# Kernel optimization log

Measured on AMD Instinct MI355X. Metric: run time of the kernel, lower is better.

The kernel has to match this reference:

```python
import jax, jax.numpy as jnp
import numpy as np

HEADS = 16
HEAD_DIM = 64  # qk_dim(1024) // heads(16)
SCALE = HEAD_DIM ** (-0.5)


def setup_inputs() -> dict:
    key = jax.random.key(0)
    k1, k2, k3, k4 = jax.random.split(key, 4)
    b, n, d = 2, 2048, 1024
    x = jax.random.normal(k1, (b, n, d), dtype=jnp.float32)
    mask = jax.random.randint(k2, (1, 1, n, n), 0, 2, dtype=jnp.int32)
    W_qkv = jax.random.normal(k3, (d, 3 * d), dtype=jnp.float32) * (d ** -0.5)
    W_out = jax.random.normal(k4, (d, d), dtype=jnp.float32) * (d ** -0.5)
    b_out = jnp.zeros((d,), dtype=jnp.float32)
    return {"x": x, "mask": mask, "W_qkv": W_qkv, "W_out": W_out, "b_out": b_out}


def reference(x, mask, W_qkv, W_out, b_out):
    b, n, d = x.shape
    qkv = x @ W_qkv  # [b, n, 3d]
    q, k, v = jnp.split(qkv, 3, axis=-1)

    def to_heads(t):
        return t.reshape(b, n, HEADS, HEAD_DIM).transpose(0, 2, 1, 3)  # b h n d

    q, k, v = to_heads(q), to_heads(k), to_heads(v)
    attn = jnp.einsum('bhid,bhjd->bhij', q, k) * SCALE
    attn = jnp.where(mask == 0, jnp.float32(-1e9), attn)
    attn = jax.nn.softmax(attn, axis=-1)
    out = jnp.einsum('bhij,bhjd->bhid', attn, v)  # b h n d
    out = out.transpose(0, 2, 1, 3).reshape(b, n, d)  # b n (h d)
    return out @ W_out + b_out
```

## Files before the change

kernel.cpp:

```cpp
#include <hip/hip_runtime.h>
#include <hip/hip_bf16.h>

typedef __bf16 bf16x8 __attribute__((ext_vector_type(8)));
typedef float f32x4 __attribute__((ext_vector_type(4)));
typedef float f32x16 __attribute__((ext_vector_type(16)));
typedef unsigned short u16;
typedef unsigned int u32;
typedef unsigned long long u64;
typedef u32 u32x4v __attribute__((ext_vector_type(4)));

#define QSCALE 0.18033688011112042f

__device__ __forceinline__ u16 f2b(float x) {
  __hip_bfloat16 h = __float2bfloat16(x);
  return __builtin_bit_cast(u16, h);
}

__device__ __forceinline__ float exp2_fast(float x) {
#if __has_builtin(__builtin_amdgcn_exp2f)
  return __builtin_amdgcn_exp2f(x);
#else
  float r; asm("v_exp_f32 %0, %1" : "=v"(r) : "v"(x)); return r;
#endif
}

__device__ __forceinline__ void gload_lds16(const void* g, void* l) {
  __builtin_amdgcn_global_load_lds((const __attribute__((address_space(1))) u32*)g,
                                   (__attribute__((address_space(3))) u32*)l, 16, 0, 0);
}

__global__ __launch_bounds__(256) void cast_bf16_kernel(const float* __restrict__ src,
                                                        u16* __restrict__ dst, int n4) {
  int i = blockIdx.x * 256 + threadIdx.x;
  if (i >= n4) return;
  float4 v = ((const float4*)src)[i];
  ushort4 o;
  o.x = f2b(v.x); o.y = f2b(v.y); o.z = f2b(v.z); o.w = f2b(v.w);
  ((ushort4*)dst)[i] = o;
}

__global__ __launch_bounds__(256) void transpose_cast_kernel(const float* __restrict__ src,
                                                             u16* __restrict__ dst,
                                                             int R, int C) {
  __shared__ float t[32][33];
  int c0 = blockIdx.x * 32, r0 = blockIdx.y * 32;
  int tx = threadIdx.x, ty = threadIdx.y;
  for (int k = 0; k < 32; k += 8)
    t[ty + k][tx] = src[(size_t)(r0 + ty + k) * C + c0 + tx];
  __syncthreads();
  for (int k = 0; k < 32; k += 8)
    dst[(size_t)(c0 + ty + k) * R + r0 + tx] = f2b(t[tx][ty + k]);
}

__global__ __launch_bounds__(256) void maskbits_kernel(const int* __restrict__ mask,
                                                       u64* __restrict__ bits) {
  int gtid = blockIdx.x * 256 + threadIdx.x;
  int wid = gtid >> 6, lane = gtid & 63;
  int v = mask[(size_t)wid * 64 + lane];
  u64 b = __ballot(v != 0);
  if (lane == 0) bits[wid] = b;
}

__global__ __launch_bounds__(256) void gemm_qkv_kernel(const u16* __restrict__ A,
                                                       const u16* __restrict__ Bt,
                                                       u16* __restrict__ Qb,
                                                       u16* __restrict__ Kb,
                                                       u16* __restrict__ Vt) {
  __shared__ u16 lA[128 * 32], lB[128 * 32];
  const int tid = threadIdx.x, lane = tid & 63, w = tid >> 6;
  const int wr = w >> 1, wc = w & 1, lrow = lane & 15, lk = lane >> 4;
  const int bm = blockIdx.y, bn = blockIdx.x;
  const int srow = tid >> 2, scol = (tid & 3) * 8;
  const u16* Arow = A + (size_t)(bm * 128 + srow) * 1024 + scol;
  const u16* Brow = Bt + (size_t)(bn * 128 + srow) * 1024 + scol;
  f32x4 acc[4][4] = {};
  for (int k0 = 0; k0 < 1024; k0 += 32) {
    __syncthreads();
    gload_lds16(Arow + k0,             (char*)lA + w * 1024);
    gload_lds16(Arow + 64 * 1024 + k0, (char*)lA + 4096 + w * 1024);
    gload_lds16(Brow + k0,             (char*)lB + w * 1024);
    gload_lds16(Brow + 64 * 1024 + k0, (char*)lB + 4096 + w * 1024);
    __syncthreads();
    bf16x8 af[4], bfr[4];
    for (int mi = 0; mi < 4; mi++)
      af[mi] = *(const bf16x8*)&lA[(wr * 64 + mi * 16 + lrow) * 32 + lk * 8];
    for (int ni = 0; ni < 4; ni++)
      bfr[ni] = *(const bf16x8*)&lB[(wc * 64 + ni * 16 + lrow) * 32 + lk * 8];
    for (int mi = 0; mi < 4; mi++)
      for (int ni = 0; ni < 4; ni++)
        acc[mi][ni] = __builtin_amdgcn_mfma_f32_16x16x32_bf16(af[mi], bfr[ni], acc[mi][ni], 0, 0, 0);
  }
  const int rowbase = bm * 128 + wr * 64;
  const int colbase = bn * 128 + wc * 64;
  for (int mi = 0; mi < 4; mi++)
    for (int ni = 0; ni < 4; ni++)
      for (int r = 0; r < 4; r++) {
        int row = rowbase + mi * 16 + lk * 4 + r;
        int col = colbase + ni * 16 + lrow;
        int b = row >> 11, n = row & 2047;
        int which = col >> 10, within = col & 1023;
        int h = within >> 6, d = within & 63;
        float av = acc[mi][ni][r];
        size_t bh = (size_t)(b * 16 + h);
        if (which == 0)      Qb[(bh * 2048 + n) * 64 + d] = f2b(av * QSCALE);
        else if (which == 1) Kb[(bh * 2048 + n) * 64 + d] = f2b(av);
        else                 Vt[(bh * 64 + d) * 2048 + n] = f2b(av);
      }
}

__global__ __launch_bounds__(256) void gemm_out_kernel(const u16* __restrict__ A,
                                                       const u16* __restrict__ Bt,
                                                       const float* __restrict__ bias,
                                                       float* __restrict__ out) {
  __shared__ u16 lA[128 * 32], lB[128 * 32];
  const int tid = threadIdx.x, lane = tid & 63, w = tid >> 6;
  const int wr = w >> 1, wc = w & 1, lrow = lane & 15, lk = lane >> 4;
  const int bm = blockIdx.y, bn = blockIdx.x;
  const int srow = tid >> 2, scol = (tid & 3) * 8;
  const u16* Arow = A + (size_t)(bm * 128 + srow) * 1024 + scol;
  const u16* Brow = Bt + (size_t)(bn * 128 + srow) * 1024 + scol;
  f32x4 acc[4][4] = {};
  for (int k0 = 0; k0 < 1024; k0 += 32) {
    __syncthreads();
    gload_lds16(Arow + k0,             (char*)lA + w * 1024);
    gload_lds16(Arow + 64 * 1024 + k0, (char*)lA + 4096 + w * 1024);
    gload_lds16(Brow + k0,             (char*)lB + w * 1024);
    gload_lds16(Brow + 64 * 1024 + k0, (char*)lB + 4096 + w * 1024);
    __syncthreads();
    bf16x8 af[4], bfr[4];
    for (int mi = 0; mi < 4; mi++)
      af[mi] = *(const bf16x8*)&lA[(wr * 64 + mi * 16 + lrow) * 32 + lk * 8];
    for (int ni = 0; ni < 4; ni++)
      bfr[ni] = *(const bf16x8*)&lB[(wc * 64 + ni * 16 + lrow) * 32 + lk * 8];
    for (int mi = 0; mi < 4; mi++)
      for (int ni = 0; ni < 4; ni++)
        acc[mi][ni] = __builtin_amdgcn_mfma_f32_16x16x32_bf16(af[mi], bfr[ni], acc[mi][ni], 0, 0, 0);
  }
  const int rowbase = bm * 128 + wr * 64;
  const int colbase = bn * 128 + wc * 64;
  for (int mi = 0; mi < 4; mi++)
    for (int ni = 0; ni < 4; ni++)
      for (int r = 0; r < 4; r++) {
        int row = rowbase + mi * 16 + lk * 4 + r;
        int col = colbase + ni * 16 + lrow;
        out[(size_t)row * 1024 + col] = acc[mi][ni][r] + bias[col];
      }
}

__global__ __launch_bounds__(256, 3) void attn_kernel(const u16* __restrict__ Qb,
                                                      const u16* __restrict__ Kb,
                                                      const u16* __restrict__ Vt,
                                                      const u64* __restrict__ Mb,
                                                      u16* __restrict__ attnb) {
  __shared__ u16 Klds[2][64 * 64];
  __shared__ u16 Vlds[2][64 * 64];
  __shared__ u32 Plds[4][32 * 32];
  const int tid = threadIdx.x, lane = tid & 63, w = tid >> 6;
  const int l31 = lane & 31, hi = lane >> 5;
  const int qt = blockIdx.x, bh = blockIdx.y;
  const int h = bh & 15, b = bh >> 4;
  const int q = qt * 128 + w * 32 + l31;
  const u16* Qp = Qb + (size_t)bh * 2048 * 64;
  const u16* Kp = Kb + (size_t)bh * 2048 * 64;
  const u16* Vp = Vt + (size_t)bh * 64 * 2048;
  const u64* Mrow = Mb + (size_t)q * 32;
  u32* myP = &Plds[w][0];

  const int rsub = lane >> 3;
  const int usrc = ((lane & 7) ^ rsub) * 8;
  auto stage = [&](int bi, int j0) {
#pragma unroll
    for (int j = 0; j < 2; j++) {
      const int i = w * 2 + j;
      const int row = 8 * i + rsub;
      gload_lds16(Kp + (size_t)(j0 + row) * 64 + usrc, (char*)&Klds[bi][0] + i * 1024);
      gload_lds16(Vp + (size_t)row * 2048 + j0 + usrc, (char*)&Vlds[bi][0] + i * 1024);
    }
  };

  bf16x8 qf[4];
#pragma unroll
  for (int t = 0; t < 4; t++)
    qf[t] = *(const bf16x8*)&Qp[(size_t)q * 64 + t * 16 + hi * 8];

  f32x16 acc0 = {}, acc1 = {};
  float m_run = -3.0e38f, lsum = 0.f;

  stage(0, 0);
  u64 mw = Mrow[0];
  int cur = 0;

  for (int c = 0; c < 32; c++) {
    __syncthreads();
    if (c + 1 < 32) stage(cur ^ 1, (c + 1) * 64);
    u64 mw_n = (c + 1 < 32) ? Mrow[c + 1] : 0;

    bf16x8 kc[2][4];
#pragma unroll
    for (int t2 = 0; t2 < 2; t2++)
#pragma unroll
      for (int t = 0; t < 4; t++) {
        const int row = t2 * 32 + l31;
        const int u = (t * 2 + hi) ^ (l31 & 7);
        kc[t2][t] = *(const bf16x8*)((const char*)&Klds[cur][0] + row * 128 + u * 16);
      }

    f32x16 s0 = {}, s1 = {};
    __builtin_amdgcn_s_setprio(1);
#pragma unroll
    for (int t = 0; t < 4; t++) {
      s0 = __builtin_amdgcn_mfma_f32_32x32x16_bf16(kc[0][t], qf[t], s0, 0, 0, 0);
      s1 = __builtin_amdgcn_mfma_f32_32x32x16_bf16(kc[1][t], qf[t], s1, 0, 0, 0);
    }
    __builtin_amdgcn_s_setprio(0);

    bf16x8 va[2][4];
#pragma unroll
    for (int dt = 0; dt < 2; dt++)
#pragma unroll
      for (int kk = 0; kk < 4; kk++) {
        const int row = dt * 32 + l31;
        const int u = (kk * 2 + hi) ^ (l31 & 7);
        va[dt][kk] = *(const bf16x8*)((const char*)&Vlds[cur][0] + row * 128 + u * 16);
      }

    float mx[8];
#pragma unroll
    for (int i = 0; i < 8; i++)
      mx[i] = fmaxf(fmaxf(s0[i], s0[i + 8]), fmaxf(s1[i], s1[i + 8]));
    float m01 = fmaxf(mx[0], mx[1]), m23 = fmaxf(mx[2], mx[3]);
    float m45 = fmaxf(mx[4], mx[5]), m67 = fmaxf(mx[6], mx[7]);
    float pm = fmaxf(fmaxf(m01, m23), fmaxf(m45, m67));
    pm = fmaxf(pm, __shfl_xor(pm, 32, 64));

    if (__any(pm > m_run + 8.f)) {
      float mn = fmaxf(m_run, pm);
      float fs = exp2_fast(m_run - mn);
      m_run = mn;
      lsum *= fs;
      acc0 *= fs;
      acc1 *= fs;
    }

    u32 w0s = (u32)(mw >> (4 * hi));
    u32 w1s = (u32)((mw >> 32) >> (4 * hi));
#pragma unroll
    for (int p = 0; p < 8; p++) {
      const int r0 = 2 * p;
      const int sh = (r0 & 3) + 8 * (p >> 1);
      const int wrow = (p & 1) + 4 * (p >> 1) + 2 * hi;
      float a0 = exp2_fast(s0[r0] - m_run);
      float a1 = exp2_fast(s0[r0 + 1] - m_run);
      float b0 = exp2_fast(s1[r0] - m_run);
      float b1 = exp2_fast(s1[r0 + 1] - m_run);
      a0 = ((w0s >> sh) & 1u) ? a0 : 0.f;
      a1 = ((w0s >> (sh + 1)) & 1u) ? a1 : 0.f;
      b0 = ((w1s >> sh) & 1u) ? b0 : 0.f;
      b1 = ((w1s >> (sh + 1)) & 1u) ? b1 : 0.f;
      lsum += (a0 + a1) + (b0 + b1);
      myP[wrow * 32 + l31]        = (u32)f2b(a0) | ((u32)f2b(a1) << 16);
      myP[(wrow + 16) * 32 + l31] = (u32)f2b(b0) | ((u32)f2b(b1) << 16);
    }

    asm volatile("s_waitcnt lgkmcnt(0)" ::: "memory");
    __builtin_amdgcn_s_setprio(1);
#pragma unroll
    for (int kk = 0; kk < 4; kk++) {
      const int base = (kk * 8 + hi * 4) * 32 + l31;
      u32 r0 = myP[base];
      u32 r1 = myP[base + 32];
      u32 r2 = myP[base + 64];
      u32 r3 = myP[base + 96];
      u32x4v pv4 = {r0, r1, r2, r3};
      bf16x8 pbf = __builtin_bit_cast(bf16x8, pv4);
      acc0 = __builtin_amdgcn_mfma_f32_32x32x16_bf16(va[0][kk], pbf, acc0, 0, 0, 0);
      acc1 = __builtin_amdgcn_mfma_f32_32x32x16_bf16(va[1][kk], pbf, acc1, 0, 0, 0);
    }
    __builtin_amdgcn_s_setprio(0);

    mw = mw_n;
    cur ^= 1;
  }

  lsum += __shfl_xor(lsum, 32, 64);
  float inv = 1.0f / lsum;
  u16* orow = attnb + ((size_t)b * 2048 + q) * 1024 + h * 64;
#pragma unroll
  for (int rq = 0; rq < 4; rq++) {
    const int rb = rq * 4;
    {
      u32 lo = (u32)f2b(acc0[rb] * inv) | ((u32)f2b(acc0[rb + 1] * inv) << 16);
      u32 hi2 = (u32)f2b(acc0[rb + 2] * inv) | ((u32)f2b(acc0[rb + 3] * inv) << 16);
      uint2 st; st.x = lo; st.y = hi2;
      *(uint2*)(orow + 8 * rq + 4 * hi) = st;
    }
    {
      u32 lo = (u32)f2b(acc1[rb] * inv) | ((u32)f2b(acc1[rb + 1] * inv) << 16);
      u32 hi2 = (u32)f2b(acc1[rb + 2] * inv) | ((u32)f2b(acc1[rb + 3] * inv) << 16);
      uint2 st; st.x = lo; st.y = hi2;
      *(uint2*)(orow + 32 + 8 * rq + 4 * hi) = st;
    }
  }
}

extern "C" void kernel_launch(void* const* d_in, const int* in_sizes, int n_in,
                              void* d_out, int out_size, void* d_ws, size_t ws_size,
                              hipStream_t stream) {
  const float* x    = (const float*)d_in[0];
  const int*   mask = (const int*)d_in[1];
  const float* Wqkv = (const float*)d_in[2];
  const float* Wout = (const float*)d_in[3];
  const float* bout = (const float*)d_in[4];
  float* out = (float*)d_out;

  char* ws = (char*)d_ws;
  u16* xb     = (u16*)(ws);
  u16* attnb  = xb;
  u16* Wqkv_t = (u16*)(ws + (size_t)(8u << 20));
  u16* Wout_t = Wqkv_t;
  u64* mbits  = (u64*)(ws + (size_t)(10u << 20));
  u16* Qb     = (u16*)(ws + (size_t)(14u << 20));
  u16* Kb     = (u16*)(ws + (size_t)(22u << 20));
  u16* Vt     = (u16*)(ws + (size_t)(30u << 20));

  cast_bf16_kernel<<<4096, 256, 0, stream>>>(x, xb, 4096 * 1024 / 4);
  transpose_cast_kernel<<<dim3(96, 32), dim3(32, 8), 0, stream>>>(Wqkv, Wqkv_t, 1024, 3072);
  gemm_qkv_kernel<<<dim3(24, 32), 256, 0, stream>>>(xb, Wqkv_t, Qb, Kb, Vt);
  transpose_cast_kernel<<<dim3(32, 32), dim3(32, 8), 0, stream>>>(Wout, Wout_t, 1024, 1024);
  maskbits_kernel<<<16384, 256, 0, stream>>>(mask, mbits);
  attn_kernel<<<dim3(16, 32), 256, 0, stream>>>(Qb, Kb, Vt, mbits, attnb);
  gemm_out_kernel<<<dim3(8, 32), 256, 0, stream>>>(attnb, Wout_t, bout, out);
}
```

Baseline: 163.2 us.

## Split attention KV range across two blocks and merge partials

Splits the 2048-key loop of the attention kernel into two halves across a new grid z dimension. That doubles the block count from 512 to 1024 for better occupancy on the many CUs. Each half writes unnormalized bf16 partial outputs plus running max and sum. A new merge kernel rescales and combines them into the final attention output. This adds extra global traffic, an extra launch, and bf16 rounding of the unnormalized partials.

```diff
diff --git a/kernel.cpp b/kernel.cpp
--- a/kernel.cpp
+++ b/kernel.cpp
@@ -14,6 +14,11 @@
 __device__ __forceinline__ u16 f2b(float x) {
   __hip_bfloat16 h = __float2bfloat16(x);
   return __builtin_bit_cast(u16, h);
+}
+
+__device__ __forceinline__ float b2f(u16 x) {
+  u32 u = ((u32)x) << 16;
+  return __builtin_bit_cast(float, u);
 }
 
 __device__ __forceinline__ float exp2_fast(float x) {
@@ -151,15 +156,16 @@
                                                       const u16* __restrict__ Kb,
                                                       const u16* __restrict__ Vt,
                                                       const u64* __restrict__ Mb,
-                                                      u16* __restrict__ attnb) {
+                                                      u16* __restrict__ accP,
+                                                      float2* __restrict__ ml) {
   __shared__ u16 Klds[2][64 * 64];
   __shared__ u16 Vlds[2][64 * 64];
   __shared__ u32 Plds[4][32 * 32];
   const int tid = threadIdx.x, lane = tid & 63, w = tid >> 6;
   const int l31 = lane & 31, hi = lane >> 5;
-  const int qt = blockIdx.x, bh = blockIdx.y;
-  const int h = bh & 15, b = bh >> 4;
+  const int qt = blockIdx.x, bh = blockIdx.y, z = blockIdx.z;
   const int q = qt * 128 + w * 32 + l31;
+  const int kv0 = z << 10;
   const u16* Qp = Qb + (size_t)bh * 2048 * 64;
   const u16* Kp = Kb + (size_t)bh * 2048 * 64;
   const u16* Vp = Vt + (size_t)bh * 64 * 2048;
@@ -186,14 +192,15 @@
   f32x16 acc0 = {}, acc1 = {};
   float m_run = -3.0e38f, lsum = 0.f;
 
-  stage(0, 0);
-  u64 mw = Mrow[0];
+  stage(0, kv0);
+  u64 mw = Mrow[kv0 >> 6];
   int cur = 0;
 
-  for (int c = 0; c < 32; c++) {
-    __syncthreads();
-    if (c + 1 < 32) stage(cur ^ 1, (c + 1) * 64);
-    u64 mw_n = (c + 1 < 32) ? Mrow[c + 1] : 0;
+  for (int c = 0; c < 16; c++) {
+    const int j0 = kv0 + c * 64;
+    __syncthreads();
+    if (c + 1 < 16) stage(cur ^ 1, j0 + 64);
+    u64 mw_n = (c + 1 < 16) ? Mrow[(j0 >> 6) + 1] : 0;
 
     bf16x8 kc[2][4];
 #pragma unroll
@@ -283,24 +290,49 @@
   }
 
   lsum += __shfl_xor(lsum, 32, 64);
-  float inv = 1.0f / lsum;
-  u16* orow = attnb + ((size_t)b * 2048 + q) * 1024 + h * 64;
+  const size_t row = (size_t)z * 32 * 2048 + (size_t)bh * 2048 + q;
+  u16* ap = accP + row * 64;
 #pragma unroll
   for (int rq = 0; rq < 4; rq++) {
     const int rb = rq * 4;
     {
-      u32 lo = (u32)f2b(acc0[rb] * inv) | ((u32)f2b(acc0[rb + 1] * inv) << 16);
-      u32 hi2 = (u32)f2b(acc0[rb + 2] * inv) | ((u32)f2b(acc0[rb + 3] * inv) << 16);
+      u32 lo = (u32)f2b(acc0[rb]) | ((u32)f2b(acc0[rb + 1]) << 16);
+      u32 hi2 = (u32)f2b(acc0[rb + 2]) | ((u32)f2b(acc0[rb + 3]) << 16);
       uint2 st; st.x = lo; st.y = hi2;
-      *(uint2*)(orow + 8 * rq + 4 * hi) = st;
+      *(uint2*)(ap + 8 * rq + 4 * hi) = st;
     }
     {
-      u32 lo = (u32)f2b(acc1[rb] * inv) | ((u32)f2b(acc1[rb + 1] * inv) << 16);
-      u32 hi2 = (u32)f2b(acc1[rb + 2] * inv) | ((u32)f2b(acc1[rb + 3] * inv) << 16);
+      u32 lo = (u32)f2b(acc1[rb]) | ((u32)f2b(acc1[rb + 1]) << 16);
+      u32 hi2 = (u32)f2b(acc1[rb + 2]) | ((u32)f2b(acc1[rb + 3]) << 16);
       uint2 st; st.x = lo; st.y = hi2;
-      *(uint2*)(orow + 32 + 8 * rq + 4 * hi) = st;
+      *(uint2*)(ap + 32 + 8 * rq + 4 * hi) = st;
     }
   }
+  if (hi == 0) ml[row] = make_float2(m_run, lsum);
+}
+
+__global__ __launch_bounds__(256) void attn_merge_kernel(const u16* __restrict__ accP,
+                                                         const float2* __restrict__ ml,
+                                                         u16* __restrict__ attnb) {
+  const int gid = blockIdx.x * 256 + threadIdx.x;
+  const int row = gid >> 4;
+  const int dq = gid & 15;
+  const size_t Z = (size_t)32 * 2048;
+  float2 mlA = ml[row], mlB = ml[Z + row];
+  float mT = fmaxf(mlA.x, mlB.x);
+  float fA = exp2_fast(mlA.x - mT), fB = exp2_fast(mlB.x - mT);
+  float inv = 1.0f / (mlA.y * fA + mlB.y * fB);
+  fA *= inv; fB *= inv;
+  const u16* pA = accP + (size_t)row * 64 + dq * 4;
+  const u16* pB = pA + Z * 64;
+  ushort4 a = *(const ushort4*)pA, bv = *(const ushort4*)pB;
+  ushort4 o;
+  o.x = f2b(b2f(a.x) * fA + b2f(bv.x) * fB);
+  o.y = f2b(b2f(a.y) * fA + b2f(bv.y) * fB);
+  o.z = f2b(b2f(a.z) * fA + b2f(bv.z) * fB);
+  o.w = f2b(b2f(a.w) * fA + b2f(bv.w) * fB);
+  const int bh = row >> 11, q = row & 2047, b = bh >> 4, h = bh & 15;
+  *(ushort4*)(attnb + ((size_t)b * 2048 + q) * 1024 + h * 64 + dq * 4) = o;
 }
 
 extern "C" void kernel_launch(void* const* d_in, const int* in_sizes, int n_in,
@@ -322,12 +354,15 @@
   u16* Qb     = (u16*)(ws + (size_t)(14u << 20));
   u16* Kb     = (u16*)(ws + (size_t)(22u << 20));
   u16* Vt     = (u16*)(ws + (size_t)(30u << 20));
+  u16* accP   = (u16*)(ws + (size_t)(38u << 20));
+  float2* ml  = (float2*)(ws + (size_t)(55u << 20));
 
   cast_bf16_kernel<<<4096, 256, 0, stream>>>(x, xb, 4096 * 1024 / 4);
   transpose_cast_kernel<<<dim3(96, 32), dim3(32, 8), 0, stream>>>(Wqkv, Wqkv_t, 1024, 3072);
   gemm_qkv_kernel<<<dim3(24, 32), 256, 0, stream>>>(xb, Wqkv_t, Qb, Kb, Vt);
   transpose_cast_kernel<<<dim3(32, 32), dim3(32, 8), 0, stream>>>(Wout, Wout_t, 1024, 1024);
   maskbits_kernel<<<16384, 256, 0, stream>>>(mask, mbits);
-  attn_kernel<<<dim3(16, 32), 256, 0, stream>>>(Qb, Kb, Vt, mbits, attnb);
+  attn_kernel<<<dim3(16, 32, 2), 256, 0, stream>>>(Qb, Kb, Vt, mbits, accP, ml);
+  attn_merge_kernel<<<4096, 256, 0, stream>>>(accP, ml, attnb);
   gemm_out_kernel<<<dim3(8, 32), 256, 0, stream>>>(attnb, Wout_t, bout, out);
 }
```

New measurement: 168.6 us. 3.3% more time.

## Split attention KV range across wave pairs and merge partial softmax states

Applied to the files above, without the earlier changes.

Each block now covers 64 queries instead of 128, and four waves form two query groups times two key halves. Each wave computes scores for 32 keys per tile, and the P operand is built in registers through cross-lane shuffles instead of an LDS round trip. At the end the two key-half partial results (max, sum, accumulators) are merged through shared memory. The grid doubles to 1024 blocks, which improves CU fill, at the cost of reloading K/V tiles per 64 queries, an extra merge step, and a lower occupancy hint.

```diff
diff --git a/kernel.cpp b/kernel.cpp
--- a/kernel.cpp
+++ b/kernel.cpp
@@ -147,24 +147,22 @@
       }
 }
 
-__global__ __launch_bounds__(256, 3) void attn_kernel(const u16* __restrict__ Qb,
+__global__ __launch_bounds__(256, 2) void attn_kernel(const u16* __restrict__ Qb,
                                                       const u16* __restrict__ Kb,
                                                       const u16* __restrict__ Vt,
                                                       const u64* __restrict__ Mb,
                                                       u16* __restrict__ attnb) {
-  __shared__ u16 Klds[2][64 * 64];
-  __shared__ u16 Vlds[2][64 * 64];
-  __shared__ u32 Plds[4][32 * 32];
+  __shared__ u32 smem[8192];
   const int tid = threadIdx.x, lane = tid & 63, w = tid >> 6;
   const int l31 = lane & 31, hi = lane >> 5;
+  const int wq = w & 1, wk = w >> 1;
   const int qt = blockIdx.x, bh = blockIdx.y;
   const int h = bh & 15, b = bh >> 4;
-  const int q = qt * 128 + w * 32 + l31;
+  const int q = qt * 64 + wq * 32 + l31;
   const u16* Qp = Qb + (size_t)bh * 2048 * 64;
   const u16* Kp = Kb + (size_t)bh * 2048 * 64;
   const u16* Vp = Vt + (size_t)bh * 64 * 2048;
   const u64* Mrow = Mb + (size_t)q * 32;
-  u32* myP = &Plds[w][0];
 
   const int rsub = lane >> 3;
   const int usrc = ((lane & 7) ^ rsub) * 8;
@@ -173,8 +171,8 @@
     for (int j = 0; j < 2; j++) {
       const int i = w * 2 + j;
       const int row = 8 * i + rsub;
-      gload_lds16(Kp + (size_t)(j0 + row) * 64 + usrc, (char*)&Klds[bi][0] + i * 1024);
-      gload_lds16(Vp + (size_t)row * 2048 + j0 + usrc, (char*)&Vlds[bi][0] + i * 1024);
+      gload_lds16(Kp + (size_t)(j0 + row) * 64 + usrc, (char*)smem + bi * 8192 + i * 1024);
+      gload_lds16(Vp + (size_t)row * 2048 + j0 + usrc, (char*)smem + 16384 + bi * 8192 + i * 1024);
     }
   };
 
@@ -195,39 +193,27 @@
     if (c + 1 < 32) stage(cur ^ 1, (c + 1) * 64);
     u64 mw_n = (c + 1 < 32) ? Mrow[c + 1] : 0;
 
-    bf16x8 kc[2][4];
-#pragma unroll
-    for (int t2 = 0; t2 < 2; t2++)
-#pragma unroll
-      for (int t = 0; t < 4; t++) {
-        const int row = t2 * 32 + l31;
-        const int u = (t * 2 + hi) ^ (l31 & 7);
-        kc[t2][t] = *(const bf16x8*)((const char*)&Klds[cur][0] + row * 128 + u * 16);
-      }
-
-    f32x16 s0 = {}, s1 = {};
+    const char* Kbase = (const char*)smem + cur * 8192;
+    const char* Vbase = (const char*)smem + 16384 + cur * 8192;
+
+    bf16x8 kc[4];
+#pragma unroll
+    for (int t = 0; t < 4; t++) {
+      const int row = wk * 32 + l31;
+      const int u = (t * 2 + hi) ^ (l31 & 7);
+      kc[t] = *(const bf16x8*)(Kbase + row * 128 + u * 16);
+    }
+
+    f32x16 s = {};
     __builtin_amdgcn_s_setprio(1);
 #pragma unroll
-    for (int t = 0; t < 4; t++) {
-      s0 = __builtin_amdgcn_mfma_f32_32x32x16_bf16(kc[0][t], qf[t], s0, 0, 0, 0);
-      s1 = __builtin_amdgcn_mfma_f32_32x32x16_bf16(kc[1][t], qf[t], s1, 0, 0, 0);
-    }
+    for (int t = 0; t < 4; t++)
+      s = __builtin_amdgcn_mfma_f32_32x32x16_bf16(kc[t], qf[t], s, 0, 0, 0);
     __builtin_amdgcn_s_setprio(0);
 
-    bf16x8 va[2][4];
-#pragma unroll
-    for (int dt = 0; dt < 2; dt++)
-#pragma unroll
-      for (int kk = 0; kk < 4; kk++) {
-        const int row = dt * 32 + l31;
-        const int u = (kk * 2 + hi) ^ (l31 & 7);
-        va[dt][kk] = *(const bf16x8*)((const char*)&Vlds[cur][0] + row * 128 + u * 16);
-      }
-
     float mx[8];
 #pragma unroll
-    for (int i = 0; i < 8; i++)
-      mx[i] = fmaxf(fmaxf(s0[i], s0[i + 8]), fmaxf(s1[i], s1[i + 8]));
+    for (int i = 0; i < 8; i++) mx[i] = fmaxf(s[i], s[i + 8]);
     float m01 = fmaxf(mx[0], mx[1]), m23 = fmaxf(mx[2], mx[3]);
     float m45 = fmaxf(mx[4], mx[5]), m67 = fmaxf(mx[6], mx[7]);
     float pm = fmaxf(fmaxf(m01, m23), fmaxf(m45, m67));
@@ -242,36 +228,43 @@
       acc1 *= fs;
     }
 
-    u32 w0s = (u32)(mw >> (4 * hi));
-    u32 w1s = (u32)((mw >> 32) >> (4 * hi));
+    u32 msel = wk ? (u32)(mw >> 32) : (u32)mw;
+    u32 wsh = msel >> (4 * hi);
+    u32 wwd[8];
 #pragma unroll
     for (int p = 0; p < 8; p++) {
       const int r0 = 2 * p;
       const int sh = (r0 & 3) + 8 * (p >> 1);
-      const int wrow = (p & 1) + 4 * (p >> 1) + 2 * hi;
-      float a0 = exp2_fast(s0[r0] - m_run);
-      float a1 = exp2_fast(s0[r0 + 1] - m_run);
-      float b0 = exp2_fast(s1[r0] - m_run);
-      float b1 = exp2_fast(s1[r0 + 1] - m_run);
-      a0 = ((w0s >> sh) & 1u) ? a0 : 0.f;
-      a1 = ((w0s >> (sh + 1)) & 1u) ? a1 : 0.f;
-      b0 = ((w1s >> sh) & 1u) ? b0 : 0.f;
-      b1 = ((w1s >> (sh + 1)) & 1u) ? b1 : 0.f;
-      lsum += (a0 + a1) + (b0 + b1);
-      myP[wrow * 32 + l31]        = (u32)f2b(a0) | ((u32)f2b(a1) << 16);
-      myP[(wrow + 16) * 32 + l31] = (u32)f2b(b0) | ((u32)f2b(b1) << 16);
-    }
-
-    asm volatile("s_waitcnt lgkmcnt(0)" ::: "memory");
+      float a0 = exp2_fast(s[r0] - m_run);
+      float a1 = exp2_fast(s[r0 + 1] - m_run);
+      a0 = ((wsh >> sh) & 1u) ? a0 : 0.f;
+      a1 = ((wsh >> (sh + 1)) & 1u) ? a1 : 0.f;
+      lsum += a0 + a1;
+      wwd[p] = (u32)f2b(a0) | ((u32)f2b(a1) << 16);
+    }
+
+    bf16x8 va[2][2];
+#pragma unroll
+    for (int dt = 0; dt < 2; dt++)
+#pragma unroll
+      for (int kk = 0; kk < 2; kk++) {
+        const int row = dt * 32 + l31;
+        const int u = (wk * 4 + kk * 2 + hi) ^ (l31 & 7);
+        va[dt][kk] = *(const bf16x8*)(Vbase + row * 128 + u * 16);
+      }
+
     __builtin_amdgcn_s_setprio(1);
 #pragma unroll
-    for (int kk = 0; kk < 4; kk++) {
-      const int base = (kk * 8 + hi * 4) * 32 + l31;
-      u32 r0 = myP[base];
-      u32 r1 = myP[base + 32];
-      u32 r2 = myP[base + 64];
-      u32 r3 = myP[base + 96];
-      u32x4v pv4 = {r0, r1, r2, r3};
+    for (int kk = 0; kk < 2; kk++) {
+      const int b4 = kk * 4;
+      u32 a0w = wwd[b4 + 0], a1w = wwd[b4 + 1], a2w = wwd[b4 + 2], a3w = wwd[b4 + 3];
+      u32 e0 = __shfl_xor(hi ? a0w : a2w, 32, 64);
+      u32 e1 = __shfl_xor(hi ? a1w : a3w, 32, 64);
+      u32 f0 = hi ? e0 : a0w;
+      u32 f1 = hi ? e1 : a1w;
+      u32 f2c = hi ? a2w : e0;
+      u32 f3 = hi ? a3w : e1;
+      u32x4v pv4 = {f0, f1, f2c, f3};
       bf16x8 pbf = __builtin_bit_cast(bf16x8, pv4);
       acc0 = __builtin_amdgcn_mfma_f32_32x32x16_bf16(va[0][kk], pbf, acc0, 0, 0, 0);
       acc1 = __builtin_amdgcn_mfma_f32_32x32x16_bf16(va[1][kk], pbf, acc1, 0, 0, 0);
@@ -283,22 +276,48 @@
   }
 
   lsum += __shfl_xor(lsum, 32, 64);
-  float inv = 1.0f / lsum;
-  u16* orow = attnb + ((size_t)b * 2048 + q) * 1024 + h * 64;
-#pragma unroll
-  for (int rq = 0; rq < 4; rq++) {
-    const int rb = rq * 4;
-    {
-      u32 lo = (u32)f2b(acc0[rb] * inv) | ((u32)f2b(acc0[rb + 1] * inv) << 16);
-      u32 hi2 = (u32)f2b(acc0[rb + 2] * inv) | ((u32)f2b(acc0[rb + 3] * inv) << 16);
-      uint2 st; st.x = lo; st.y = hi2;
-      *(uint2*)(orow + 8 * rq + 4 * hi) = st;
-    }
-    {
-      u32 lo = (u32)f2b(acc1[rb] * inv) | ((u32)f2b(acc1[rb + 1] * inv) << 16);
-      u32 hi2 = (u32)f2b(acc1[rb + 2] * inv) | ((u32)f2b(acc1[rb + 3] * inv) << 16);
-      uint2 st; st.x = lo; st.y = hi2;
-      *(uint2*)(orow + 32 + 8 * rq + 4 * hi) = st;
+  __syncthreads();
+  float* comb = (float*)smem;
+  float* cb = comb + wq * 34 * 64;
+  if (wk == 1) {
+    cb[0 * 64 + lane] = m_run;
+    cb[1 * 64 + lane] = lsum;
+#pragma unroll
+    for (int r = 0; r < 16; r++) {
+      cb[(2 + r) * 64 + lane]  = acc0[r];
+      cb[(18 + r) * 64 + lane] = acc1[r];
+    }
+  }
+  __syncthreads();
+  if (wk == 0) {
+    float mB = cb[0 * 64 + lane];
+    float lB_ = cb[1 * 64 + lane];
+    float mT = fmaxf(m_run, mB);
+    float fA = exp2_fast(m_run - mT);
+    float fB = exp2_fast(mB - mT);
+    float lt = lsum * fA + lB_ * fB;
+    float ia = fA / lt, ib = fB / lt;
+#pragma unroll
+    for (int r = 0; r < 16; r++) {
+      acc0[r] = acc0[r] * ia + cb[(2 + r) * 64 + lane] * ib;
+      acc1[r] = acc1[r] * ia + cb[(18 + r) * 64 + lane] * ib;
+    }
+    u16* orow = attnb + ((size_t)b * 2048 + q) * 1024 + h * 64;
+#pragma unroll
+    for (int rq = 0; rq < 4; rq++) {
+      const int rb = rq * 4;
+      {
+        u32 lo = (u32)f2b(acc0[rb]) | ((u32)f2b(acc0[rb + 1]) << 16);
+        u32 hi2 = (u32)f2b(acc0[rb + 2]) | ((u32)f2b(acc0[rb + 3]) << 16);
+        uint2 st; st.x = lo; st.y = hi2;
+        *(uint2*)(orow + 8 * rq + 4 * hi) = st;
+      }
+      {
+        u32 lo = (u32)f2b(acc1[rb]) | ((u32)f2b(acc1[rb + 1]) << 16);
+        u32 hi2 = (u32)f2b(acc1[rb + 2]) | ((u32)f2b(acc1[rb + 3]) << 16);
+        uint2 st; st.x = lo; st.y = hi2;
+        *(uint2*)(orow + 32 + 8 * rq + 4 * hi) = st;
+      }
     }
   }
 }
@@ -328,6 +347,6 @@
   gemm_qkv_kernel<<<dim3(24, 32), 256, 0, stream>>>(xb, Wqkv_t, Qb, Kb, Vt);
   transpose_cast_kernel<<<dim3(32, 32), dim3(32, 8), 0, stream>>>(Wout, Wout_t, 1024, 1024);
   maskbits_kernel<<<16384, 256, 0, stream>>>(mask, mbits);
-  attn_kernel<<<dim3(16, 32), 256, 0, stream>>>(Qb, Kb, Vt, mbits, attnb);
+  attn_kernel<<<dim3(32, 32), 256, 0, stream>>>(Qb, Kb, Vt, mbits, attnb);
   gemm_out_kernel<<<dim3(8, 32), 256, 0, stream>>>(attnb, Wout_t, bout, out);
 }
```

Result: faster. 159.4 us (-2.4%).
